# Kernel tuning notes

Measured on AMD Instinct MI355X. Metric: run time of the kernel, lower is better.

## Reference

```python
import jax, jax.numpy as jnp
import numpy as np
import math

NUM_BINS = 10
TAIL_BOUND = 5.0
FILTER_CHANNELS = 192
KERNEL_SIZE = 3
N_LAYERS = 3
HALF = 1
MIN_BIN = 1e-3
MIN_DERIV = 1e-3


def conv1d(x, w, b, dilation=1, groups=1, padding=0):
    # x: [B,C,T], w: [O, C//groups, K]
    y = jax.lax.conv_general_dilated(
        x, w, window_strides=(1,), padding=[(padding, padding)],
        rhs_dilation=(dilation,), dimension_numbers=('NCH', 'OIH', 'NCH'),
        feature_group_count=groups)
    return y + b[None, :, None]


def ln_channels(x, g, b, eps=1e-5):
    # LayerNorm over channel dim (VITS modules.LayerNorm)
    m = jnp.mean(x, axis=1, keepdims=True)
    v = jnp.mean((x - m) ** 2, axis=1, keepdims=True)
    return g[None, :, None] * (x - m) * jax.lax.rsqrt(v + eps) + b[None, :, None]


def rq_spline(x1, uw, uh, ud):
    # piecewise rational-quadratic transform with linear tails (Durkan et al.)
    # x1: [B,1,T]; uw,uh: [B,1,T,K]; ud: [B,1,T,K-1]
    K = NUM_BINS
    tb = TAIL_BOUND
    inside = (x1 >= -tb) & (x1 <= tb)

    const = math.log(math.exp(1.0 - MIN_DERIV) - 1.0)  # softplus^-1(1-min_d)
    ud = jnp.pad(ud, [(0, 0)] * (ud.ndim - 1) + [(1, 1)], constant_values=const)

    widths = jax.nn.softmax(uw, axis=-1)
    widths = MIN_BIN + (1.0 - MIN_BIN * K) * widths
    cumw = jnp.pad(jnp.cumsum(widths, -1), [(0, 0)] * (uw.ndim - 1) + [(1, 0)])
    cumw = 2.0 * tb * cumw - tb
    cumw = cumw.at[..., 0].set(-tb).at[..., -1].set(tb)
    widths = cumw[..., 1:] - cumw[..., :-1]

    heights = jax.nn.softmax(uh, axis=-1)
    heights = MIN_BIN + (1.0 - MIN_BIN * K) * heights
    cumh = jnp.pad(jnp.cumsum(heights, -1), [(0, 0)] * (uh.ndim - 1) + [(1, 0)])
    cumh = 2.0 * tb * cumh - tb
    cumh = cumh.at[..., 0].set(-tb).at[..., -1].set(tb)
    heights = cumh[..., 1:] - cumh[..., :-1]

    derivs = MIN_DERIV + jax.nn.softplus(ud)  # [..., K+1]

    xin = jnp.clip(x1, -tb, tb)  # clamp so out-of-range lanes stay finite
    locs = cumw.at[..., -1].add(1e-6)
    bin_idx = jnp.clip(jnp.sum((xin[..., None] >= locs).astype(jnp.int32), -1) - 1, 0, K - 1)

    def take(a):
        return jnp.take_along_axis(a, bin_idx[..., None], axis=-1)[..., 0]

    icw = take(cumw)
    iw = take(widths)
    ich = take(cumh)
    ih = take(heights)
    d_l = take(derivs[..., :-1])
    d_r = take(derivs[..., 1:])
    delta = ih / iw

    theta = (xin - icw) / iw
    t1m = theta * (1.0 - theta)
    numerator = ih * (delta * theta * theta + d_l * t1m)
    denominator = delta + (d_l + d_r - 2.0 * delta) * t1m
    y = ich + numerator / denominator
    dnum = (delta * delta) * (d_r * theta * theta + 2.0 * delta * t1m + d_l * (1.0 - theta) ** 2)
    lad = jnp.log(dnum) - 2.0 * jnp.log(denominator)

    out = jnp.where(inside, y, x1)       # linear tails: identity outside
    lad = jnp.where(inside, lad, 0.0)
    return out, lad


def reference(x, x_mask, pre_w, pre_b, sep_w, sep_b, pw_w, pw_b,
              ln1_g, ln1_b, ln2_g, ln2_b, proj_w, proj_b):
    x0, x1 = x[:, :HALF], x[:, HALF:]
    h = conv1d(x0, pre_w, pre_b)
    # DDSConv (dilated depth-separable conv stack), p_dropout=0
    for i in range(N_LAYERS):
        d = KERNEL_SIZE ** i
        pad = (KERNEL_SIZE * d - d) // 2
        y = conv1d(h * x_mask, sep_w[i], sep_b[i], dilation=d,
                   groups=FILTER_CHANNELS, padding=pad)
        y = jax.nn.gelu(ln_channels(y, ln1_g[i], ln1_b[i]), approximate=False)
        y = conv1d(y, pw_w[i], pw_b[i])
        y = jax.nn.gelu(ln_channels(y, ln2_g[i], ln2_b[i]), approximate=False)
        h = h + y
    h = h * x_mask
    h = conv1d(h, proj_w, proj_b) * x_mask  # [B, half*(3K-1), T]
    b, c, t = x0.shape
    h = h.reshape(b, c, -1, t).transpose(0, 1, 3, 2)  # [B, half, T, 3K-1]
    scale = math.sqrt(FILTER_CHANNELS)
    uw = h[..., :NUM_BINS] / scale
    uh = h[..., NUM_BINS:2 * NUM_BINS] / scale
    ud = h[..., 2 * NUM_BINS:]
    x1o, lad = rq_spline(x1, uw, uh, ud)
    out = jnp.concatenate([x0, x1o], axis=1) * x_mask
    logdet = jnp.sum(lad * x_mask, axis=(1, 2))
    return out, logdet


def setup_inputs() -> dict:
    key = jax.random.key(0)
    ks = jax.random.split(key, 8)
    B, T, C, L, K = 64, 4096, FILTER_CHANNELS, N_LAYERS, KERNEL_SIZE
    return {
        'x': jax.random.normal(ks[0], (B, 2, T), jnp.float32),
        'x_mask': jnp.ones((B, 1, T), jnp.float32),
        'pre_w': jax.random.normal(ks[1], (C, 1, 1), jnp.float32) * 0.1,
        'pre_b': jnp.zeros((C,), jnp.float32),
        'sep_w': jax.random.normal(ks[2], (L, C, 1, K), jnp.float32) * 0.1,
        'sep_b': jnp.zeros((L, C), jnp.float32),
        'pw_w': jax.random.normal(ks[3], (L, C, C, 1), jnp.float32) * (1.0 / np.sqrt(C).astype(np.float32)),
        'pw_b': jnp.zeros((L, C), jnp.float32),
        'ln1_g': jnp.ones((L, C), jnp.float32),
        'ln1_b': jnp.zeros((L, C), jnp.float32),
        'ln2_g': jnp.ones((L, C), jnp.float32),
        'ln2_b': jnp.zeros((L, C), jnp.float32),
        'proj_w': jax.random.normal(ks[4], (HALF * (3 * NUM_BINS - 1), C, 1), jnp.float32) * 0.01,
        'proj_b': jnp.zeros((HALF * (3 * NUM_BINS - 1),), jnp.float32),
    }
```

## Files before the change

### kernel.cpp

```cpp
#include <hip/hip_runtime.h>
#include <stdint.h>

#define TT_ 4096
#define CC_ 192
#define TILE_ 64
#define HALO_ 13
#define TW_ 90
#define HS_ 100
#define YTS_ 200
#define NT_ 512

typedef float f32x2 __attribute__((ext_vector_type(2)));
typedef float f32x4 __attribute__((ext_vector_type(4)));
typedef short s16x4 __attribute__((ext_vector_type(4)));
typedef short s16x8 __attribute__((ext_vector_type(8)));
typedef uint32_t ui32x2 __attribute__((ext_vector_type(2)));
typedef uint32_t ui32x4 __attribute__((ext_vector_type(4)));

__device__ __forceinline__ float bf2f(short s){
  uint32_t u = ((uint32_t)(uint16_t)s) << 16;
  float f; __builtin_memcpy(&f, &u, 4); return f;
}
__device__ __forceinline__ float bfhalf(uint32_t u, int hi){
  uint32_t v = hi ? (u & 0xFFFF0000u) : (u << 16);
  float f; __builtin_memcpy(&f, &v, 4); return f;
}
__device__ __forceinline__ short f2bf(float f){
  uint32_t u; __builtin_memcpy(&u, &f, 4);
  u += 0x7FFFu + ((u >> 16) & 1u);
  return (short)(u >> 16);
}
__device__ __forceinline__ uint32_t fbits(float f){
  uint32_t u; __builtin_memcpy(&u, &f, 4); return u;
}
__device__ __forceinline__ uint32_t pk_trunc(float lo, float hi){
  return __builtin_amdgcn_perm(fbits(hi), fbits(lo), 0x07060302u);
}
__device__ __forceinline__ uint32_t rne_u(float f){
  uint32_t u = fbits(f);
  return u + 0x7FFFu + ((u >> 16) & 1u);
}
__device__ __forceinline__ uint32_t pk_rne(float lo, float hi){
  return __builtin_amdgcn_perm(rne_u(hi), rne_u(lo), 0x07060302u);
}
__device__ __forceinline__ f32x2 pfma(f32x2 a, f32x2 b, f32x2 c){
  return __builtin_elementwise_fma(a, b, c);
}
__device__ __forceinline__ f32x2 gelu2(f32x2 x){
  f32x2 s = x*x;
  f32x2 t = pfma(s, f32x2{0.0713548162f,0.0713548162f}, f32x2{1.5957691216f,1.5957691216f});
  f32x2 p = x*t;
  f32x2 q = p * f32x2{-1.44269504089f,-1.44269504089f};
  f32x2 e; e[0] = __builtin_amdgcn_exp2f(q[0]); e[1] = __builtin_amdgcn_exp2f(q[1]);
  f32x2 d = e + f32x2{1.f,1.f};
  f32x2 r; r[0] = __builtin_amdgcn_rcpf(d[0]); r[1] = __builtin_amdgcn_rcpf(d[1]);
  return x*r;
}
__device__ __forceinline__ int ytix(int row, int col){
  int key = (row ^ (row >> 2)) & 3;
  return row*YTS_ + ((((col >> 3) ^ key) << 3) | (col & 7));
}

template<int D>
__device__ __forceinline__ void dw_pass(const short* __restrict__ Hs, short* __restrict__ YTs,
    const float* __restrict__ sw, const float* __restrict__ sb,
    int jlo, int jhi, int tid){
  constexpr int WO = (D==9) ? 16 : 8;
  constexpr int NU = (D==9) ? 20 : 12;
  for (int g = tid; g < 96*12; g += NT_){
    int cg = g % 96, jg = g / 96;
    int j0 = jg*8;
    if (j0 + 8 <= jlo || j0 >= jhi) continue;
    int c0 = cg*2;
    uint32_t wpa[NU], wpb[NU];
    {
      const uint32_t* ra = (const uint32_t*)(Hs + (c0+0)*HS_ + j0 - WO);
      const uint32_t* rb = (const uint32_t*)(Hs + (c0+1)*HS_ + j0 - WO);
      #pragma unroll
      for (int u = 0; u < NU/2; ++u){
        ui32x2 ta = *(const ui32x2*)(ra + u*2);
        ui32x2 tb = *(const ui32x2*)(rb + u*2);
        wpa[u*2] = ta[0]; wpa[u*2+1] = ta[1];
        wpb[u*2] = tb[0]; wpb[u*2+1] = tb[1];
      }
    }
    f32x2 wv0 = { sw[c0*3+0], sw[c0*3+3] };
    f32x2 wv1 = { sw[c0*3+1], sw[c0*3+4] };
    f32x2 wv2 = { sw[c0*3+2], sw[c0*3+5] };
    f32x2 bb2 = { sb[c0], sb[c0+1] };
    #pragma unroll
    for (int j = 0; j < 8; ++j){
      int h0 = WO + j - D, h1 = WO + j, h2 = WO + j + D;
      f32x2 t0 = { bfhalf(wpa[h0>>1], h0&1), bfhalf(wpb[h0>>1], h0&1) };
      f32x2 t1 = { bfhalf(wpa[h1>>1], h1&1), bfhalf(wpb[h1>>1], h1&1) };
      f32x2 t2 = { bfhalf(wpa[h2>>1], h2&1), bfhalf(wpb[h2>>1], h2&1) };
      f32x2 acc = pfma(wv0, t0, pfma(wv1, t1, pfma(wv2, t2, bb2)));
      *(uint32_t*)(YTs + ytix(j0+j, c0)) = pk_trunc(acc[0], acc[1]);
    }
  }
}

__device__ __forceinline__ void ln_stats(const short* __restrict__ YTs, float* __restrict__ SM,
                                         float* __restrict__ SR, int jlo, int jhi, int tid){
  if (tid < 384){
    int row = tid >> 2, qtr = tid & 3;
    if (row >= jlo && row < jhi){
      f32x2 s2 = {0.f,0.f}, q2 = {0.f,0.f};
      #pragma unroll
      for (int u=0;u<6;++u){
        ui32x4 w = *(const ui32x4*)(YTs + ytix(row, qtr*48 + u*8));
        #pragma unroll
        for (int k=0;k<4;++k){
          f32x2 pr = { bfhalf(w[k],0), bfhalf(w[k],1) };
          s2 += pr; q2 = pfma(pr, pr, q2);
        }
      }
      float s = s2[0]+s2[1], q = q2[0]+q2[1];
      s += __shfl_xor(s,1); q += __shfl_xor(q,1);
      s += __shfl_xor(s,2); q += __shfl_xor(q,2);
      if (qtr==0){
        float mean = s*(1.f/192.f);
        float var = fmaxf(q*(1.f/192.f) - mean*mean, 0.f);
        SM[row]=mean; SR[row]=rsqrtf(var+1e-5f);
      }
    }
  }
}

__global__ __launch_bounds__(512, 4)
void convflow_main(
    const float* __restrict__ x, const float* __restrict__ xmask,
    const float* __restrict__ pre_w, const float* __restrict__ pre_b,
    const float* __restrict__ sep_w, const float* __restrict__ sep_b,
    const float* __restrict__ pw_b,
    const float* __restrict__ ln1_g, const float* __restrict__ ln1_b,
    const float* __restrict__ ln2_g, const float* __restrict__ ln2_b,
    const float* __restrict__ proj_b,
    const short* __restrict__ Wbf, const short* __restrict__ Pbf,
    float* __restrict__ out, float* __restrict__ part)
{
  __shared__ __align__(16) char smem_raw[78592];
  float* MB = (float*)(smem_raw + 0);
  float* SP = (float*)(smem_raw + 640);
  float* SM = (float*)(smem_raw + 1024);
  float* SR = (float*)(smem_raw + 1408);
  short* H  = (short*)(smem_raw + 1792);
  short* YT = (short*)(smem_raw + 40192);
  float* HP = (float*)(smem_raw + 65792);

  const int tid = threadIdx.x;
  const int b = blockIdx.y, tile = blockIdx.x;
  const int t0 = tile*TILE_ - HALO_;

  for (int idx = tid; idx < 160; idx += NT_){
    int j = idx - 16; int t = t0 + j;
    float m = 0.f;
    if (j >= 0 && j < TW_ && t >= 0 && t < TT_) m = xmask[b*TT_ + t];
    MB[idx] = m;
  }
  for (int g = tid; g < CC_*24; g += NT_){
    int jq = g % 24, c = g / 24;
    int j0 = jq*4;
    float w = pre_w[c], bb = pre_b[c];
    float v[4];
    #pragma unroll
    for (int e=0;e<4;e++){
      int j = j0+e, t = t0+j;
      float xv = 0.f, mv = 0.f;
      if (j < TW_ && t >= 0 && t < TT_){ xv = x[(b*2)*TT_ + t]; mv = xmask[b*TT_ + t]; }
      v[e] = (w*xv + bb)*mv;
    }
    ui32x2 o; o[0] = pk_rne(v[0], v[1]); o[1] = pk_rne(v[2], v[3]);
    *(ui32x2*)(H + c*HS_ + j0) = o;
  }
  __syncthreads();

  #pragma unroll 1
  for (int li = 0; li < 3; ++li){
    const int jlo = (li==0) ? 1 : ((li==1) ? 4 : 13);
    const int jhi = (li==0) ? 89 : ((li==1) ? 86 : 77);
    const float* sw = sep_w + li*CC_*3;
    const float* sb = sep_b + li*CC_;

    if (li == 0)      dw_pass<1>(H, YT, sw, sb, jlo, jhi, tid);
    else if (li == 1) dw_pass<3>(H, YT, sw, sb, jlo, jhi, tid);
    else              dw_pass<9>(H, YT, sw, sb, jlo, jhi, tid);
    __syncthreads();

    ln_stats(YT, SM, SR, jlo, jhi, tid); __syncthreads();

    {
      const float* g1 = ln1_g + li*CC_;
      const float* b1 = ln1_b + li*CC_;
      int g = tid;
      int ch = g % 24, row = g / 24;
      short* p = YT + ytix(row, ch*8);
      ui32x4 v = *(ui32x4*)p;
      #pragma unroll 1
      while (g < 2304){
        int gn = g + NT_;
        short* pn = p; ui32x4 vn = v; int chn = ch, rown = row;
        if (gn < 2304){
          chn = gn % 24; rown = gn / 24;
          pn = YT + ytix(rown, chn*8);
          vn = *(ui32x4*)pn;
        }
        if (row >= jlo && row < jhi){
          float m = SM[row], r = SR[row];
          f32x2 r2 = {r, r}, nm2 = {-m, -m};
          f32x4 ga = *(const f32x4*)&g1[ch*8], gb = *(const f32x4*)&g1[ch*8+4];
          f32x4 ba = *(const f32x4*)&b1[ch*8], bb = *(const f32x4*)&b1[ch*8+4];
          ui32x4 o;
          #pragma unroll
          for (int k=0;k<4;++k){
            f32x2 pr = { bfhalf(v[k],0), bfhalf(v[k],1) };
            f32x2 gk = (k<2) ? f32x2{ga[2*k], ga[2*k+1]} : f32x2{gb[2*k-4], gb[2*k-3]};
            f32x2 bk = (k<2) ? f32x2{ba[2*k], ba[2*k+1]} : f32x2{bb[2*k-4], bb[2*k-3]};
            f32x2 A = gk * r2;
            f32x2 B = pfma(A, nm2, bk);
            f32x2 val = pfma(pr, A, B);
            f32x2 gl = gelu2(val);
            o[k] = pk_trunc(gl[0], gl[1]);
          }
          *(ui32x4*)p = o;
        } else {
          ui32x4 z = {0u,0u,0u,0u};
          *(ui32x4*)p = z;
        }
        g = gn; ch = chn; row = rown; p = pn; v = vn;
      }
    }
    __syncthreads();

    {
      int w = tid >> 6, lane = tid & 63, l16 = lane & 15, q = lane >> 4;
      int Mh = w & 3, Nh = w >> 2;
      f32x4 acc[3][3];
      #pragma unroll
      for (int r=0;r<3;r++)
        #pragma unroll
        for (int s=0;s<3;s++){ f32x4 z = {0.f,0.f,0.f,0.f}; acc[r][s] = z; }
      const short* Wl = Wbf + li*CC_*CC_;
      #pragma unroll
      for (int kk=0;kk<6;++kk){
        s16x8 bv[3], av[3];
        #pragma unroll
        for (int s=0;s<3;++s)
          bv[s] = *(const s16x8*)&YT[ytix((Nh*3+s)*16 + l16, kk*32 + q*8)];
        #pragma unroll
        for (int r=0;r<3;++r)
          av[r] = *(const s16x8*)&Wl[((Mh*3+r)*16 + l16)*CC_ + kk*32 + q*8];
        #pragma unroll
        for (int r=0;r<3;++r)
          #pragma unroll
          for (int s=0;s<3;++s)
            acc[r][s] = __builtin_amdgcn_mfma_f32_16x16x32_bf16(av[r], bv[s], acc[r][s], 0, 0, 0);
      }
      __syncthreads();
      #pragma unroll
      for (int r=0;r<3;++r){
        int m0 = (Mh*3+r)*16 + q*4;
        f32x4 bias = *(const f32x4*)&pw_b[li*CC_ + m0];
        #pragma unroll
        for (int s=0;s<3;++s){
          int n = (Nh*3+s)*16 + l16;
          ui32x2 ov;
          ov[0] = pk_trunc(acc[r][s][0]+bias[0], acc[r][s][1]+bias[1]);
          ov[1] = pk_trunc(acc[r][s][2]+bias[2], acc[r][s][3]+bias[3]);
          *(ui32x2*)(YT + ytix(n, m0)) = ov;
        }
      }
      __syncthreads();
    }

    ln_stats(YT, SM, SR, jlo, jhi, tid); __syncthreads();

    {
      const float* g2 = ln2_g + li*CC_;
      const float* b2 = ln2_b + li*CC_;
      int g = tid;
      int jq = g % 24, cq = g / 24;
      s16x4 y0 = *(s16x4*)(YT + ytix(jq*4+0, cq*4));
      s16x4 y1 = *(s16x4*)(YT + ytix(jq*4+1, cq*4));
      s16x4 y2 = *(s16x4*)(YT + ytix(jq*4+2, cq*4));
      s16x4 y3 = *(s16x4*)(YT + ytix(jq*4+3, cq*4));
      #pragma unroll 1
      while (g < 1152){
        int gn = g + NT_;
        int jqn = jq, cqn = cq;
        s16x4 y0n = y0, y1n = y1, y2n = y2, y3n = y3;
        if (gn < 1152){
          jqn = gn % 24; cqn = gn / 24;
          y0n = *(s16x4*)(YT + ytix(jqn*4+0, cqn*4));
          y1n = *(s16x4*)(YT + ytix(jqn*4+1, cqn*4));
          y2n = *(s16x4*)(YT + ytix(jqn*4+2, cqn*4));
          y3n = *(s16x4*)(YT + ytix(jqn*4+3, cqn*4));
        }
        int j0 = jq*4, c0 = cq*4;
        if (!(j0 + 4 <= jlo || j0 >= jhi)){
          f32x4 mv = *(f32x4*)&SM[j0], rv = *(f32x4*)&SR[j0];
          f32x4 mk = *(f32x4*)&MB[16 + j0];
          f32x4 gv = *(const f32x4*)&g2[c0], bv = *(const f32x4*)&b2[c0];
          s16x4 yr[4] = { y0, y1, y2, y3 };
          bool ok0 = (j0   >= jlo) && (j0   < jhi);
          bool ok1 = (j0+1 >= jlo) && (j0+1 < jhi);
          bool ok2 = (j0+2 >= jlo) && (j0+2 < jhi);
          bool ok3 = (j0+3 >= jlo) && (j0+3 < jhi);
          #pragma unroll
          for (int cc=0;cc<4;++cc){
            short* hp_ = H + (c0+cc)*HS_ + j0;
            ui32x2 hw = *(ui32x2*)hp_;
            f32x2 gcc = { gv[cc], gv[cc] }, bcc = { bv[cc], bv[cc] };
            ui32x2 ho;
            #pragma unroll
            for (int pp=0; pp<2; ++pp){
              int ja = pp*2, jb = ja+1;
              f32x2 pr = { bf2f(yr[ja][cc]), bf2f(yr[jb][cc]) };
              f32x2 A = f32x2{rv[ja], rv[jb]} * gcc;
              f32x2 B = pfma(A, f32x2{-mv[ja], -mv[jb]}, bcc);
              f32x2 val = pfma(pr, A, B);
              f32x2 gl = gelu2(val);
              f32x2 h2 = { bfhalf(hw[pp],0), bfhalf(hw[pp],1) };
              f32x2 hn = (h2 + gl) * f32x2{mk[ja], mk[jb]};
              bool oa = pp ? ok2 : ok0, ob = pp ? ok3 : ok1;
              float f0 = oa ? hn[0] : h2[0];
              float f1 = ob ? hn[1] : h2[1];
              ho[pp] = pk_rne(f0, f1);
            }
            *(ui32x2*)hp_ = ho;
          }
        }
        g = gn; jq = jqn; cq = cqn; y0 = y0n; y1 = y1n; y2 = y2n; y3 = y3n;
      }
    }
    __syncthreads();
  }

  {
    int w = tid >> 6;
    if (w < 4){
      int lane = tid & 63, l16 = lane & 15, q = lane >> 4;
      int mt = w >> 1, ntp = w & 1;
      f32x4 pacc[2];
      { f32x4 z = {0.f,0.f,0.f,0.f}; pacc[0] = z; pacc[1] = z; }
      #pragma unroll
      for (int kk=0;kk<6;++kk){
        s16x8 a = *(const s16x8*)&Pbf[(mt*16 + l16)*CC_ + kk*32 + q*8];
        #pragma unroll
        for (int s=0;s<2;++s){
          int n = (ntp*2+s)*16 + l16;
          s16x8 bvv;
          #pragma unroll
          for (int i=0;i<8;++i)
            bvv[i] = H[(kk*32 + q*8 + i)*HS_ + HALO_ + n];
          pacc[s] = __builtin_amdgcn_mfma_f32_16x16x32_bf16(a, bvv, pacc[s], 0, 0, 0);
        }
      }
      #pragma unroll
      for (int s=0;s<2;++s)
        #pragma unroll
        for (int e=0;e<4;e++){
          int m = mt*16 + q*4 + e;
          if (m < 29){
            int n = (ntp*2+s)*16 + l16;
            HP[n*33 + m] = (pacc[s][e] + proj_b[m]) * MB[16 + HALO_ + n];
          }
        }
    }
  }
  __syncthreads();

  float lsum_p = 0.f;
  if (tid < 128){
    const int n = tid >> 1, half = tid & 1;
    const int tg = tile*TILE_ + n;
    const float msk = MB[16 + HALO_ + n];
    const float* hp = &HP[n*33];
    const float inv_s = 0.07216878364870323f;

    const float x1v = x[(b*2+1)*TT_ + tg];
    const float xin = fminf(fmaxf(x1v, -5.f), 5.f);

    float cum[11];
    {
      float u[10];
      #pragma unroll
      for (int k=0;k<10;k++) u[k] = hp[half*10 + k]*inv_s;
      float mx = u[0];
      #pragma unroll
      for (int k=1;k<10;k++) mx = fmaxf(mx, u[k]);
      float ex[10]; float ss = 0.f;
      #pragma unroll
      for (int k=0;k<10;k++){ ex[k] = __expf(u[k]-mx); ss += ex[k]; }
      float inv = 1.0f/ss;
      cum[0] = -5.f; float cw = 0.f;
      #pragma unroll
      for (int k=0;k<10;k++){ float wk = 0.001f + 0.99f*(ex[k]*inv); cw += wk; cum[k+1] = 10.f*cw - 5.f; }
      cum[10] = 5.f;
    }
    int bin = 0;
    float dv[11];
    if (half == 0){
      int cnt = 0;
      #pragma unroll
      for (int k=0;k<11;k++){
        float lk = cum[k] + ((k==10) ? 1e-6f : 0.f);
        cnt += (xin >= lk) ? 1 : 0;
      }
      bin = cnt - 1;
      bin = (bin < 0) ? 0 : ((bin > 9) ? 9 : bin);
    } else {
      dv[0] = 1.0f; dv[10] = 1.0f;
      #pragma unroll
      for (int k=0;k<9;k++){
        float u = hp[20+k];
        float sp = (u > 15.f) ? u : log1pf(__expf(u));
        dv[k+1] = 0.001f + sp;
      }
    }
    int binx = __shfl_xor(bin, 1);
    float s0 = 0.f, s1 = 1.f, s2 = 1.f, s3 = 1.f;
    if (half == 1){
      bin = binx;
      #pragma unroll
      for (int k=0;k<10;k++){
        if (bin == k){
          s0 = cum[k]; s1 = cum[k+1]-cum[k];
          s2 = dv[k];  s3 = dv[k+1];
        }
      }
    } else {
      #pragma unroll
      for (int k=0;k<10;k++){
        if (bin == k){ s0 = cum[k]; s1 = cum[k+1]-cum[k]; }
      }
    }
    float r0 = __shfl_xor(s0,1), r1 = __shfl_xor(s1,1);
    float r2 = __shfl_xor(s2,1), r3 = __shfl_xor(s3,1);
    if (half == 0){
      float icw = s0, iw = s1, ich = r0, ih = r1, dl = r2, dr = r3;
      float delta = ih/iw;
      float th = (xin - icw)/iw;
      float t1m = th*(1.f-th);
      float num = ih*(delta*th*th + dl*t1m);
      float den = delta + (dl + dr - 2.f*delta)*t1m;
      float yv = ich + num/den;
      float omt = 1.f - th;
      float dnum = delta*delta*(dr*th*th + 2.f*delta*t1m + dl*omt*omt);
      float lad = logf(dnum) - 2.f*logf(den);
      bool inside = (x1v >= -5.f) && (x1v <= 5.f);
      float outv = inside ? yv : x1v;
      float ladv = inside ? lad : 0.f;
      out[(b*2+1)*TT_ + tg] = outv * msk;
      lsum_p = ladv * msk;
    } else {
      out[(b*2)*TT_ + tg] = x[(b*2)*TT_ + tg] * msk;
    }
  }
  #pragma unroll
  for (int off = 32; off > 0; off >>= 1) lsum_p += __shfl_xor(lsum_p, off);
  if (tid < 128 && (tid & 63) == 0) SP[tid >> 6] = lsum_p;
  __syncthreads();
  if (tid == 0) part[b*64 + tile] = SP[0] + SP[1];
}

__global__ void convflow_pre(const float* __restrict__ pw_w, const float* __restrict__ proj_w,
                             short* __restrict__ Wbf, short* __restrict__ Pbf){
  int idx = blockIdx.x*256 + threadIdx.x;
  if (idx < 110592) Wbf[idx] = f2bf(pw_w[idx]);
  if (idx < 32*192){
    int m = idx / 192, k = idx - m*192;
    Pbf[idx] = (m < 29) ? f2bf(proj_w[m*192 + k]) : (short)0;
  }
}

__global__ void convflow_logdet(const float* __restrict__ part, float* __restrict__ out){
  int bb = blockIdx.x, k = threadIdx.x;
  float s = part[bb*64 + k];
  #pragma unroll
  for (int off = 32; off > 0; off >>= 1) s += __shfl_xor(s, off);
  if (k == 0) out[524288 + bb] = s;
}

extern "C" void kernel_launch(void* const* d_in, const int* in_sizes, int n_in,
                              void* d_out, int out_size, void* d_ws, size_t ws_size,
                              hipStream_t stream) {
  const float* x      = (const float*)d_in[0];
  const float* xmask  = (const float*)d_in[1];
  const float* pre_w  = (const float*)d_in[2];
  const float* pre_b  = (const float*)d_in[3];
  const float* sep_w  = (const float*)d_in[4];
  const float* sep_b  = (const float*)d_in[5];
  const float* pw_w   = (const float*)d_in[6];
  const float* pw_b   = (const float*)d_in[7];
  const float* ln1_g  = (const float*)d_in[8];
  const float* ln1_b  = (const float*)d_in[9];
  const float* ln2_g  = (const float*)d_in[10];
  const float* ln2_b  = (const float*)d_in[11];
  const float* proj_w = (const float*)d_in[12];
  const float* proj_b = (const float*)d_in[13];

  short* Wbf = (short*)d_ws;
  short* Pbf = (short*)((char*)d_ws + 221184);
  float* part = (float*)((char*)d_ws + 233472);
  float* out = (float*)d_out;

  convflow_pre<<<432, 256, 0, stream>>>(pw_w, proj_w, Wbf, Pbf);
  dim3 grid(64, 64);
  convflow_main<<<grid, NT_, 0, stream>>>(x, xmask, pre_w, pre_b, sep_w, sep_b, pw_b,
                                          ln1_g, ln1_b, ln2_g, ln2_b, proj_b,
                                          Wbf, Pbf, out, part);
  convflow_logdet<<<64, 64, 0, stream>>>(part, out);
}
```

Before: 703.2 us.

## Store residual in time-major layout and drop YT swizzle for vectorized LDS access

The residual buffer moves from channel-major [C][100] to time-major [T][200] bf16, matching the layout of YT, and the XOR swizzle on YT indexing is removed. The depthwise conv, pre-conv, LN1 and LN2+GELU+residual passes all become one 16-byte vector per row per 8 channels. The final projection's B operand becomes a single 16-byte load instead of eight scalar strided LDS reads. The aim is fewer and wider LDS transactions and simpler indexing. Without the swizzle, MFMA operand loads from the padded 200-element rows may hit more LDS bank conflicts.

```diff
diff --git a/kernel.cpp b/kernel.cpp
--- a/kernel.cpp
+++ b/kernel.cpp
@@ -6,8 +6,7 @@
 #define TILE_ 64
 #define HALO_ 13
 #define TW_ 90
-#define HS_ 100
-#define YTS_ 200
+#define RS_ 200
 #define NT_ 512
 
 typedef float f32x2 __attribute__((ext_vector_type(2)));
@@ -56,51 +55,45 @@
   f32x2 r; r[0] = __builtin_amdgcn_rcpf(d[0]); r[1] = __builtin_amdgcn_rcpf(d[1]);
   return x*r;
 }
-__device__ __forceinline__ int ytix(int row, int col){
-  int key = (row ^ (row >> 2)) & 3;
-  return row*YTS_ + ((((col >> 3) ^ key) << 3) | (col & 7));
-}
 
 template<int D>
-__device__ __forceinline__ void dw_pass(const short* __restrict__ Hs, short* __restrict__ YTs,
+__device__ __forceinline__ void dw_pass(const short* __restrict__ R, short* __restrict__ YT,
     const float* __restrict__ sw, const float* __restrict__ sb,
     int jlo, int jhi, int tid){
-  constexpr int WO = (D==9) ? 16 : 8;
-  constexpr int NU = (D==9) ? 20 : 12;
-  for (int g = tid; g < 96*12; g += NT_){
-    int cg = g % 96, jg = g / 96;
-    int j0 = jg*8;
-    if (j0 + 8 <= jlo || j0 >= jhi) continue;
-    int c0 = cg*2;
-    uint32_t wpa[NU], wpb[NU];
-    {
-      const uint32_t* ra = (const uint32_t*)(Hs + (c0+0)*HS_ + j0 - WO);
-      const uint32_t* rb = (const uint32_t*)(Hs + (c0+1)*HS_ + j0 - WO);
-      #pragma unroll
-      for (int u = 0; u < NU/2; ++u){
-        ui32x2 ta = *(const ui32x2*)(ra + u*2);
-        ui32x2 tb = *(const ui32x2*)(rb + u*2);
-        wpa[u*2] = ta[0]; wpa[u*2+1] = ta[1];
-        wpb[u*2] = tb[0]; wpb[u*2+1] = tb[1];
-      }
-    }
-    f32x2 wv0 = { sw[c0*3+0], sw[c0*3+3] };
-    f32x2 wv1 = { sw[c0*3+1], sw[c0*3+4] };
-    f32x2 wv2 = { sw[c0*3+2], sw[c0*3+5] };
-    f32x2 bb2 = { sb[c0], sb[c0+1] };
+  for (int g = tid; g < 96*24; g += NT_){
+    int o = g % 24, j = g / 24;
+    int c0 = o*8;
+    short* dst = YT + j*RS_ + c0;
+    if (j < jlo || j >= jhi){
+      ui32x4 z = {0u,0u,0u,0u};
+      *(ui32x4*)dst = z;
+      continue;
+    }
+    ui32x4 ta = *(const ui32x4*)(R + (j-D)*RS_ + c0);
+    ui32x4 tb = *(const ui32x4*)(R + j*RS_ + c0);
+    ui32x4 tc = *(const ui32x4*)(R + (j+D)*RS_ + c0);
+    float swv[24];
     #pragma unroll
-    for (int j = 0; j < 8; ++j){
-      int h0 = WO + j - D, h1 = WO + j, h2 = WO + j + D;
-      f32x2 t0 = { bfhalf(wpa[h0>>1], h0&1), bfhalf(wpb[h0>>1], h0&1) };
-      f32x2 t1 = { bfhalf(wpa[h1>>1], h1&1), bfhalf(wpb[h1>>1], h1&1) };
-      f32x2 t2 = { bfhalf(wpa[h2>>1], h2&1), bfhalf(wpb[h2>>1], h2&1) };
-      f32x2 acc = pfma(wv0, t0, pfma(wv1, t1, pfma(wv2, t2, bb2)));
-      *(uint32_t*)(YTs + ytix(j0+j, c0)) = pk_trunc(acc[0], acc[1]);
-    }
-  }
-}
-
-__device__ __forceinline__ void ln_stats(const short* __restrict__ YTs, float* __restrict__ SM,
+    for (int u=0;u<6;++u) *(f32x4*)&swv[u*4] = *(const f32x4*)(sw + c0*3 + u*4);
+    f32x4 sba = *(const f32x4*)(sb + c0), sbb = *(const f32x4*)(sb + c0 + 4);
+    ui32x4 ov;
+    #pragma unroll
+    for (int p=0;p<4;++p){
+      f32x2 w0 = { swv[6*p+0], swv[6*p+3] };
+      f32x2 w1 = { swv[6*p+1], swv[6*p+4] };
+      f32x2 w2 = { swv[6*p+2], swv[6*p+5] };
+      f32x2 bb = (p<2) ? f32x2{ sba[2*p], sba[2*p+1] } : f32x2{ sbb[2*p-4], sbb[2*p-3] };
+      f32x2 va = { bfhalf(ta[p],0), bfhalf(ta[p],1) };
+      f32x2 vb = { bfhalf(tb[p],0), bfhalf(tb[p],1) };
+      f32x2 vc = { bfhalf(tc[p],0), bfhalf(tc[p],1) };
+      f32x2 acc = pfma(w0, va, pfma(w1, vb, pfma(w2, vc, bb)));
+      ov[p] = pk_trunc(acc[0], acc[1]);
+    }
+    *(ui32x4*)dst = ov;
+  }
+}
+
+__device__ __forceinline__ void ln_stats(const short* __restrict__ YT, float* __restrict__ SM,
                                          float* __restrict__ SR, int jlo, int jhi, int tid){
   if (tid < 384){
     int row = tid >> 2, qtr = tid & 3;
@@ -108,7 +101,7 @@
       f32x2 s2 = {0.f,0.f}, q2 = {0.f,0.f};
       #pragma unroll
       for (int u=0;u<6;++u){
-        ui32x4 w = *(const ui32x4*)(YTs + ytix(row, qtr*48 + u*8));
+        ui32x4 w = *(const ui32x4*)(YT + row*RS_ + qtr*48 + u*8);
         #pragma unroll
         for (int k=0;k<4;++k){
           f32x2 pr = { bfhalf(w[k],0), bfhalf(w[k],1) };
@@ -141,10 +134,11 @@
 {
   __shared__ __align__(16) char smem_raw[78592];
   float* MB = (float*)(smem_raw + 0);
+  float* XB = (float*)(smem_raw + 640);
   float* SP = (float*)(smem_raw + 640);
   float* SM = (float*)(smem_raw + 1024);
   float* SR = (float*)(smem_raw + 1408);
-  short* H  = (short*)(smem_raw + 1792);
+  short* R  = (short*)(smem_raw + 1792);
   short* YT = (short*)(smem_raw + 40192);
   float* HP = (float*)(smem_raw + 65792);
 
@@ -158,20 +152,29 @@
     if (j >= 0 && j < TW_ && t >= 0 && t < TT_) m = xmask[b*TT_ + t];
     MB[idx] = m;
   }
-  for (int g = tid; g < CC_*24; g += NT_){
-    int jq = g % 24, c = g / 24;
-    int j0 = jq*4;
-    float w = pre_w[c], bb = pre_b[c];
-    float v[4];
+  if (tid < 96){
+    int t = t0 + tid; float v = 0.f;
+    if (tid < TW_ && t >= 0 && t < TT_) v = x[(b*2)*TT_ + t];
+    XB[tid] = v;
+  }
+  __syncthreads();
+
+  for (int g = tid; g < 96*24; g += NT_){
+    int o = g % 24, j = g / 24;
+    int c0 = o*8;
+    float xv = XB[j], m = MB[16+j];
+    float xm = xv * m;
+    f32x4 wa = *(const f32x4*)(pre_w + c0), wb = *(const f32x4*)(pre_w + c0 + 4);
+    f32x4 ba = *(const f32x4*)(pre_b + c0), bb = *(const f32x4*)(pre_b + c0 + 4);
+    ui32x4 ov;
     #pragma unroll
-    for (int e=0;e<4;e++){
-      int j = j0+e, t = t0+j;
-      float xv = 0.f, mv = 0.f;
-      if (j < TW_ && t >= 0 && t < TT_){ xv = x[(b*2)*TT_ + t]; mv = xmask[b*TT_ + t]; }
-      v[e] = (w*xv + bb)*mv;
-    }
-    ui32x2 o; o[0] = pk_rne(v[0], v[1]); o[1] = pk_rne(v[2], v[3]);
-    *(ui32x2*)(H + c*HS_ + j0) = o;
+    for (int p=0;p<4;++p){
+      f32x2 w2 = (p<2) ? f32x2{wa[2*p], wa[2*p+1]} : f32x2{wb[2*p-4], wb[2*p-3]};
+      f32x2 b2 = (p<2) ? f32x2{ba[2*p], ba[2*p+1]} : f32x2{bb[2*p-4], bb[2*p-3]};
+      f32x2 v = pfma(w2, f32x2{xm, xm}, b2 * f32x2{m, m});
+      ov[p] = pk_rne(v[0], v[1]);
+    }
+    *(ui32x4*)(R + j*RS_ + c0) = ov;
   }
   __syncthreads();
 
@@ -182,9 +185,9 @@
     const float* sw = sep_w + li*CC_*3;
     const float* sb = sep_b + li*CC_;
 
-    if (li == 0)      dw_pass<1>(H, YT, sw, sb, jlo, jhi, tid);
-    else if (li == 1) dw_pass<3>(H, YT, sw, sb, jlo, jhi, tid);
-    else              dw_pass<9>(H, YT, sw, sb, jlo, jhi, tid);
+    if (li == 0)      dw_pass<1>(R, YT, sw, sb, jlo, jhi, tid);
+    else if (li == 1) dw_pass<3>(R, YT, sw, sb, jlo, jhi, tid);
+    else              dw_pass<9>(R, YT, sw, sb, jlo, jhi, tid);
     __syncthreads();
 
     ln_stats(YT, SM, SR, jlo, jhi, tid); __syncthreads();
@@ -192,42 +195,29 @@
     {
       const float* g1 = ln1_g + li*CC_;
       const float* b1 = ln1_b + li*CC_;
-      int g = tid;
-      int ch = g % 24, row = g / 24;
-      short* p = YT + ytix(row, ch*8);
-      ui32x4 v = *(ui32x4*)p;
-      #pragma unroll 1
-      while (g < 2304){
-        int gn = g + NT_;
-        short* pn = p; ui32x4 vn = v; int chn = ch, rown = row;
-        if (gn < 2304){
-          chn = gn % 24; rown = gn / 24;
-          pn = YT + ytix(rown, chn*8);
-          vn = *(ui32x4*)pn;
-        }
-        if (row >= jlo && row < jhi){
-          float m = SM[row], r = SR[row];
-          f32x2 r2 = {r, r}, nm2 = {-m, -m};
-          f32x4 ga = *(const f32x4*)&g1[ch*8], gb = *(const f32x4*)&g1[ch*8+4];
-          f32x4 ba = *(const f32x4*)&b1[ch*8], bb = *(const f32x4*)&b1[ch*8+4];
-          ui32x4 o;
-          #pragma unroll
-          for (int k=0;k<4;++k){
-            f32x2 pr = { bfhalf(v[k],0), bfhalf(v[k],1) };
-            f32x2 gk = (k<2) ? f32x2{ga[2*k], ga[2*k+1]} : f32x2{gb[2*k-4], gb[2*k-3]};
-            f32x2 bk = (k<2) ? f32x2{ba[2*k], ba[2*k+1]} : f32x2{bb[2*k-4], bb[2*k-3]};
-            f32x2 A = gk * r2;
-            f32x2 B = pfma(A, nm2, bk);
-            f32x2 val = pfma(pr, A, B);
-            f32x2 gl = gelu2(val);
-            o[k] = pk_trunc(gl[0], gl[1]);
-          }
-          *(ui32x4*)p = o;
-        } else {
-          ui32x4 z = {0u,0u,0u,0u};
-          *(ui32x4*)p = z;
-        }
-        g = gn; ch = chn; row = rown; p = pn; v = vn;
+      for (int g = tid; g < 96*24; g += NT_){
+        int o = g % 24, row = g / 24;
+        if (row < jlo || row >= jhi) continue;
+        int c0 = o*8;
+        short* p = YT + row*RS_ + c0;
+        float m = SM[row], r = SR[row];
+        f32x2 r2 = {r, r}, nm2 = {-m, -m};
+        f32x4 ga = *(const f32x4*)&g1[c0], gb = *(const f32x4*)&g1[c0+4];
+        f32x4 ba = *(const f32x4*)&b1[c0], bb = *(const f32x4*)&b1[c0+4];
+        ui32x4 v = *(ui32x4*)p;
+        ui32x4 ov;
+        #pragma unroll
+        for (int k=0;k<4;++k){
+          f32x2 pr = { bfhalf(v[k],0), bfhalf(v[k],1) };
+          f32x2 gk = (k<2) ? f32x2{ga[2*k], ga[2*k+1]} : f32x2{gb[2*k-4], gb[2*k-3]};
+          f32x2 bk = (k<2) ? f32x2{ba[2*k], ba[2*k+1]} : f32x2{bb[2*k-4], bb[2*k-3]};
+          f32x2 A = gk * r2;
+          f32x2 B = pfma(A, nm2, bk);
+          f32x2 val = pfma(pr, A, B);
+          f32x2 gl = gelu2(val);
+          ov[k] = pk_trunc(gl[0], gl[1]);
+        }
+        *(ui32x4*)p = ov;
       }
     }
     __syncthreads();
@@ -246,7 +236,7 @@
         s16x8 bv[3], av[3];
         #pragma unroll
         for (int s=0;s<3;++s)
-          bv[s] = *(const s16x8*)&YT[ytix((Nh*3+s)*16 + l16, kk*32 + q*8)];
+          bv[s] = *(const s16x8*)&YT[((Nh*3+s)*16 + l16)*RS_ + kk*32 + q*8];
         #pragma unroll
         for (int r=0;r<3;++r)
           av[r] = *(const s16x8*)&Wl[((Mh*3+r)*16 + l16)*CC_ + kk*32 + q*8];
@@ -267,7 +257,7 @@
           ui32x2 ov;
           ov[0] = pk_trunc(acc[r][s][0]+bias[0], acc[r][s][1]+bias[1]);
           ov[1] = pk_trunc(acc[r][s][2]+bias[2], acc[r][s][3]+bias[3]);
-          *(ui32x2*)(YT + ytix(n, m0)) = ov;
+          *(ui32x2*)(YT + n*RS_ + m0) = ov;
         }
       }
       __syncthreads();
@@ -278,59 +268,32 @@
     {
       const float* g2 = ln2_g + li*CC_;
       const float* b2 = ln2_b + li*CC_;
-      int g = tid;
-      int jq = g % 24, cq = g / 24;
-      s16x4 y0 = *(s16x4*)(YT + ytix(jq*4+0, cq*4));
-      s16x4 y1 = *(s16x4*)(YT + ytix(jq*4+1, cq*4));
-      s16x4 y2 = *(s16x4*)(YT + ytix(jq*4+2, cq*4));
-      s16x4 y3 = *(s16x4*)(YT + ytix(jq*4+3, cq*4));
-      #pragma unroll 1
-      while (g < 1152){
-        int gn = g + NT_;
-        int jqn = jq, cqn = cq;
-        s16x4 y0n = y0, y1n = y1, y2n = y2, y3n = y3;
-        if (gn < 1152){
-          jqn = gn % 24; cqn = gn / 24;
-          y0n = *(s16x4*)(YT + ytix(jqn*4+0, cqn*4));
-          y1n = *(s16x4*)(YT + ytix(jqn*4+1, cqn*4));
-          y2n = *(s16x4*)(YT + ytix(jqn*4+2, cqn*4));
-          y3n = *(s16x4*)(YT + ytix(jqn*4+3, cqn*4));
-        }
-        int j0 = jq*4, c0 = cq*4;
-        if (!(j0 + 4 <= jlo || j0 >= jhi)){
-          f32x4 mv = *(f32x4*)&SM[j0], rv = *(f32x4*)&SR[j0];
-          f32x4 mk = *(f32x4*)&MB[16 + j0];
-          f32x4 gv = *(const f32x4*)&g2[c0], bv = *(const f32x4*)&b2[c0];
-          s16x4 yr[4] = { y0, y1, y2, y3 };
-          bool ok0 = (j0   >= jlo) && (j0   < jhi);
-          bool ok1 = (j0+1 >= jlo) && (j0+1 < jhi);
-          bool ok2 = (j0+2 >= jlo) && (j0+2 < jhi);
-          bool ok3 = (j0+3 >= jlo) && (j0+3 < jhi);
-          #pragma unroll
-          for (int cc=0;cc<4;++cc){
-            short* hp_ = H + (c0+cc)*HS_ + j0;
-            ui32x2 hw = *(ui32x2*)hp_;
-            f32x2 gcc = { gv[cc], gv[cc] }, bcc = { bv[cc], bv[cc] };
-            ui32x2 ho;
-            #pragma unroll
-            for (int pp=0; pp<2; ++pp){
-              int ja = pp*2, jb = ja+1;
-              f32x2 pr = { bf2f(yr[ja][cc]), bf2f(yr[jb][cc]) };
-              f32x2 A = f32x2{rv[ja], rv[jb]} * gcc;
-              f32x2 B = pfma(A, f32x2{-mv[ja], -mv[jb]}, bcc);
-              f32x2 val = pfma(pr, A, B);
-              f32x2 gl = gelu2(val);
-              f32x2 h2 = { bfhalf(hw[pp],0), bfhalf(hw[pp],1) };
-              f32x2 hn = (h2 + gl) * f32x2{mk[ja], mk[jb]};
-              bool oa = pp ? ok2 : ok0, ob = pp ? ok3 : ok1;
-              float f0 = oa ? hn[0] : h2[0];
-              float f1 = ob ? hn[1] : h2[1];
-              ho[pp] = pk_rne(f0, f1);
-            }
-            *(ui32x2*)hp_ = ho;
-          }
-        }
-        g = gn; jq = jqn; cq = cqn; y0 = y0n; y1 = y1n; y2 = y2n; y3 = y3n;
+      for (int g = tid; g < 96*24; g += NT_){
+        int o = g % 24, row = g / 24;
+        if (row < jlo || row >= jhi) continue;
+        int c0 = o*8;
+        float m = SM[row], r = SR[row], mk = MB[16+row];
+        f32x2 r2 = {r, r}, nm2 = {-m, -m}, mk2 = {mk, mk};
+        f32x4 ga = *(const f32x4*)&g2[c0], gb = *(const f32x4*)&g2[c0+4];
+        f32x4 ba = *(const f32x4*)&b2[c0], bb = *(const f32x4*)&b2[c0+4];
+        ui32x4 yv = *(ui32x4*)(YT + row*RS_ + c0);
+        short* rp = R + row*RS_ + c0;
+        ui32x4 rv = *(ui32x4*)rp;
+        ui32x4 ov;
+        #pragma unroll
+        for (int k=0;k<4;++k){
+          f32x2 pr = { bfhalf(yv[k],0), bfhalf(yv[k],1) };
+          f32x2 gk = (k<2) ? f32x2{ga[2*k], ga[2*k+1]} : f32x2{gb[2*k-4], gb[2*k-3]};
+          f32x2 bk = (k<2) ? f32x2{ba[2*k], ba[2*k+1]} : f32x2{bb[2*k-4], bb[2*k-3]};
+          f32x2 A = gk * r2;
+          f32x2 B = pfma(A, nm2, bk);
+          f32x2 val = pfma(pr, A, B);
+          f32x2 gl = gelu2(val);
+          f32x2 h2 = { bfhalf(rv[k],0), bfhalf(rv[k],1) };
+          f32x2 hn = (h2 + gl) * mk2;
+          ov[k] = pk_rne(hn[0], hn[1]);
+        }
+        *(ui32x4*)rp = ov;
       }
     }
     __syncthreads();
@@ -349,11 +312,8 @@
         #pragma unroll
         for (int s=0;s<2;++s){
           int n = (ntp*2+s)*16 + l16;
-          s16x8 bvv;
-          #pragma unroll
-          for (int i=0;i<8;++i)
-            bvv[i] = H[(kk*32 + q*8 + i)*HS_ + HALO_ + n];
-          pacc[s] = __builtin_amdgcn_mfma_f32_16x16x32_bf16(a, bvv, pacc[s], 0, 0, 0);
+          s16x8 bv = *(const s16x8*)&R[(HALO_ + n)*RS_ + kk*32 + q*8];
+          pacc[s] = __builtin_amdgcn_mfma_f32_16x16x32_bf16(a, bv, pacc[s], 0, 0, 0);
         }
       }
       #pragma unroll
```

New measurement: 621.5 us. -11.6%, faster.
